# Kernel optimization log

Measured on AMD Instinct MI355X. Metric: run time of the kernel, lower is better.

## Reference

```python
import jax, jax.numpy as jnp
import numpy as np


def setup_inputs() -> dict:
    key = jax.random.key(0)
    k1, k2, k3, k4 = jax.random.split(key, 4)
    B, T, IN, D = 32, 256, 64, 128
    x = jax.random.normal(k1, (B, T, IN), dtype=jnp.float32)
    h0 = jnp.zeros((B, D), dtype=jnp.float32)
    Wx = jax.random.normal(k2, (IN, D), dtype=jnp.float32) * 0.01
    Wgate = jax.random.normal(k3, (D, D), dtype=jnp.float32) * 0.01
    Wh = jax.random.normal(k4, (D, D), dtype=jnp.float32) * 0.01
    return {"x": x, "h0": h0, "Wx": Wx, "Wgate": Wgate, "Wh": Wh}


def reference(x, h0, Wx, Wgate, Wh):
    # x: (B, T, in_dim); h0: (B, dim); returns (h_final, y, hidden_grads, dh_dWh)
    def step_single(h_r, x_r):
        # per-sample gated update: h_r (dim,), x_r (in_dim,)
        pre = x_r @ Wx + h_r @ Wh
        a = jax.nn.gelu(pre, approximate=False)  # torch GELU() is the exact erf variant
        g = jax.nn.sigmoid(a @ Wgate)
        hn = g * h_r + (1.0 - g)
        return hn, hn

    # per-step, per-sample Jacobian d h_new / d h  (mirrors vmap(jacrev(..., argnums=1)))
    jac_batched = jax.vmap(jax.jacrev(step_single, argnums=0, has_aux=True))

    def body(h, x_t):  # h: (B, dim), x_t: (B, in_dim)
        jac, h_new = jac_batched(h, x_t)  # jac: (B, dim, dim)
        return h_new, (h_new, jac)

    xt = jnp.swapaxes(x, 0, 1)  # (T, B, in_dim)
    h_final, (ys, jacs) = jax.lax.scan(body, h0, xt)
    y = jnp.swapaxes(ys, 0, 1)  # (B, T, dim)

    # last-step Jacobian wrt Wh, evaluated with the post-update h (as in the torch code)
    x_last = x[:, -1, :]

    def f_wh(Wh_):
        pre = x_last @ Wx + h_final @ Wh_
        a = jax.nn.gelu(pre, approximate=False)
        g = jax.nn.sigmoid(a @ Wgate)
        return g * h_final + (1.0 - g)

    dh_dWh = jax.jacrev(f_wh)(Wh)  # (B, dim, dim, dim)
    return (h_final, y, jacs, dh_dWh)
```

## Files before the change

### kernel.cpp

```cpp
#include <hip/hip_runtime.h>


#define JACOFF 1052672L
#define DHWOFF 135270400L

typedef __attribute__((ext_vector_type(8))) short frag_ab;
typedef __attribute__((ext_vector_type(4))) float frag_cd;

__device__ __forceinline__ short f2bf(float f) {
    unsigned u = __builtin_bit_cast(unsigned, f);
    unsigned r = (u + 0x7fffu + ((u >> 16) & 1u)) >> 16;
    return (short)r;
}

__device__ __forceinline__ void wg_barrier() {
    asm volatile("s_waitcnt lgkmcnt(0)\n\ts_barrier" ::: "memory");
}

__device__ __forceinline__ float dpp_xor1(float x) {
    int r = __builtin_amdgcn_mov_dpp(__builtin_bit_cast(int, x), 0xB1, 0xF, 0xF, true);
    return __builtin_bit_cast(float, r);
}
__device__ __forceinline__ float dpp_xor2(float x) {
    int r = __builtin_amdgcn_mov_dpp(__builtin_bit_cast(int, x), 0x4E, 0xF, 0xF, true);
    return __builtin_bit_cast(float, r);
}

__device__ __forceinline__ void gelu_pair(float pre, float& a, float& dval) {
    const float inv_sqrt2   = 0.70710678118654752f;
    const float inv_sqrt2pi = 0.39894228040143268f;
    float ex2 = __expf(-0.5f * pre * pre);
    float az  = fabsf(pre) * inv_sqrt2;
    float t   = 1.0f / (1.0f + 0.3275911f * az);
    float poly = ((((1.061405429f * t - 1.453152027f) * t + 1.421413741f) * t
                   - 0.284496736f) * t + 0.254829592f) * t;
    float erf_abs = 1.0f - poly * ex2;
    float erf_z = (pre < 0.f) ? -erf_abs : erf_abs;
    float cdf = 0.5f * (1.0f + erf_z);
    a = pre * cdf;
    dval = cdf + pre * inv_sqrt2pi * ex2;
}

__global__ __launch_bounds__(256) void prep_xw_kernel(
    const float* __restrict__ Wh, const float* __restrict__ Wg,
    const float* __restrict__ x, const float* __restrict__ Wx,
    float* __restrict__ whT, float* __restrict__ wgT, float* __restrict__ xw)
{
    int blk = blockIdx.x;
    int tid = threadIdx.x;
    if (blk < 128) {
        int idx = blk * 256 + tid;
        if (idx < 16384) {
            int k = idx >> 7, i = idx & 127;
            whT[i * 128 + k] = Wh[idx];
        } else {
            int r = idx - 16384;
            int k = r >> 7, i = r & 127;
            wgT[i * 128 + k] = Wg[r];
        }
        return;
    }
    __shared__ float xs[2][64];
    int sub = tid >> 7;
    int bt = (blk - 128) * 2 + sub;
    int i = tid & 127;
    if (i < 64) xs[sub][i] = x[bt * 64 + i];
    __syncthreads();
    float acc = 0.f;
#pragma unroll
    for (int m = 0; m < 64; ++m)
        acc += xs[sub][m] * Wx[m * 128 + i];
    xw[bt * 128 + i] = acc;
}

__global__ __launch_bounds__(512, 1) void scan_pk_kernel(
    const float* __restrict__ xw, const float* __restrict__ h0,
    const float* __restrict__ whT, const float* __restrict__ wgT,
    const float* __restrict__ Wgate, const float* __restrict__ Wh,
    float* __restrict__ out,
    short* __restrict__ Abf, float* __restrict__ wgv, float* __restrict__ wc,
    float* __restrict__ wdF, float* __restrict__ wuF, float* __restrict__ whF,
    short* __restrict__ PT)
{
    int tid = threadIdx.x;
    if (blockIdx.x >= 32) {
        int c = (blockIdx.x - 32) * 32 + (tid >> 4);
        int k0 = (tid & 15) * 8;
        int i = c >> 7, j = c & 127;
        short v[8];
#pragma unroll
        for (int m = 0; m < 8; ++m) {
            float wg = Wgate[(k0 + m) * 128 + i];
            float wh = Wh[j * 128 + k0 + m];
            v[m] = f2bf(wg * wh);
        }
        *(frag_ab*)(PT + (long)c * 128 + k0) = *(frag_ab*)v;
        return;
    }

    const int b = blockIdx.x;
    const int i = tid >> 2, qtr = tid & 3;
    __shared__ float hbuf[2][128];
    __shared__ float abuf[128];
    float wh[32], wgc[32];
    {
        const float* whr = whT + i * 128 + qtr * 32;
        const float* wgr = wgT + i * 128 + qtr * 32;
#pragma unroll
        for (int k = 0; k < 32; k += 4) {
            float4 a4 = *(const float4*)(whr + k);
            wh[k] = a4.x; wh[k + 1] = a4.y; wh[k + 2] = a4.z; wh[k + 3] = a4.w;
            float4 b4 = *(const float4*)(wgr + k);
            wgc[k] = b4.x; wgc[k + 1] = b4.y; wgc[k + 2] = b4.z; wgc[k + 3] = b4.w;
        }
    }
    if (qtr == 0) hbuf[0][i] = h0[b * 128 + i];
    __syncthreads();

    float xwv = xw[(b * 256 + 0) * 128 + i];
    float xw1 = xw[(b * 256 + 1) * 128 + i];

    for (int t = 0; t < 256; ++t) {
        int p = t & 1;
        int tn = (t < 254) ? t + 2 : 255;
        float xw2 = xw[(b * 256 + tn) * 128 + i];

        float s0 = 0.f, s1 = 0.f, s2 = 0.f, s3 = 0.f;
        const float* hb = &hbuf[p][qtr * 32];
#pragma unroll
        for (int k = 0; k < 32; k += 4) {
            float4 h4 = *(const float4*)(hb + k);
            s0 += h4.x * wh[k];
            s1 += h4.y * wh[k + 1];
            s2 += h4.z * wh[k + 2];
            s3 += h4.w * wh[k + 3];
        }
        float s = (s0 + s1) + (s2 + s3);
        s += dpp_xor1(s);
        s += dpp_xor2(s);
        float pre = xwv + s;

        float a, dval;
        gelu_pair(pre, a, dval);

        long tb = (long)(t * 32 + b) * 128 + i;
        if (qtr == 0) {
            Abf[tb] = f2bf(dval);
            abuf[i] = a;
        }
        wg_barrier();

        float r0 = 0.f, r1 = 0.f, r2 = 0.f, r3 = 0.f;
        const float* ab = &abuf[qtr * 32];
#pragma unroll
        for (int k = 0; k < 32; k += 4) {
            float4 a4 = *(const float4*)(ab + k);
            r0 += a4.x * wgc[k];
            r1 += a4.y * wgc[k + 1];
            r2 += a4.z * wgc[k + 2];
            r3 += a4.w * wgc[k + 3];
        }
        float r = (r0 + r1) + (r2 + r3);
        r += dpp_xor1(r);
        r += dpp_xor2(r);
        float g = 1.0f / (1.0f + __expf(-r));
        float hp = hbuf[p][i];
        float c = (hp - 1.0f) * g * (1.0f - g);
        float hn = g * hp + 1.0f - g;
        if (qtr == 0) {
            hbuf[p ^ 1][i] = hn;
            wgv[tb] = g;
            wc[tb] = c;
            out[4096 + (b * 256 + t) * 128 + i] = hn;
        }
        xwv = xw1; xw1 = xw2;
        wg_barrier();
    }

    float hfin = hbuf[0][i];
    if (qtr == 0) {
        out[b * 128 + i] = hfin;
        whF[b * 128 + i] = hfin;
    }

    {
        float s0 = 0.f, s1 = 0.f, s2 = 0.f, s3 = 0.f;
        const float* hb = &hbuf[0][qtr * 32];
#pragma unroll
        for (int k = 0; k < 32; k += 4) {
            float4 h4 = *(const float4*)(hb + k);
            s0 += h4.x * wh[k];
            s1 += h4.y * wh[k + 1];
            s2 += h4.z * wh[k + 2];
            s3 += h4.w * wh[k + 3];
        }
        float s = (s0 + s1) + (s2 + s3);
        s += dpp_xor1(s);
        s += dpp_xor2(s);
        float pre = xwv + s;
        float a, dval;
        gelu_pair(pre, a, dval);
        if (qtr == 0) {
            wdF[b * 128 + i] = dval;
            abuf[i] = a;
        }
        __syncthreads();
        float r0 = 0.f, r1 = 0.f, r2 = 0.f, r3 = 0.f;
        const float* ab = &abuf[qtr * 32];
#pragma unroll
        for (int k = 0; k < 32; k += 4) {
            float4 a4 = *(const float4*)(ab + k);
            r0 += a4.x * wgc[k];
            r1 += a4.y * wgc[k + 1];
            r2 += a4.z * wgc[k + 2];
            r3 += a4.w * wgc[k + 3];
        }
        float r = (r0 + r1) + (r2 + r3);
        r += dpp_xor1(r);
        r += dpp_xor2(r);
        float g = 1.0f / (1.0f + __expf(-r));
        if (qtr == 0) wuF[b * 128 + i] = (hfin - 1.0f) * g * (1.0f - g);
    }
}

__global__ __launch_bounds__(256) void jacmm_dhdw_kernel(
    const short* __restrict__ Abf,
    const short* __restrict__ PT,
    const float* __restrict__ wgv,
    const float* __restrict__ wc,
    const float* __restrict__ Wgate,
    const float* __restrict__ dF, const float* __restrict__ uF, const float* __restrict__ hF,
    float* __restrict__ out)
{
    int bx = blockIdx.x;
    int tid = threadIdx.x;
    int grp = bx / 3, rem = bx % 3;

    if (rem == 2) {
        __shared__ float hs[128], dsh[128];
        int b = grp >> 7, i = grp & 127;
        if (tid < 128) {
            hs[tid] = hF[b * 128 + tid];
            dsh[tid] = dF[b * 128 + tid];
        }
        __syncthreads();
        float u = uF[b * 128 + i];
        int q0 = (tid & 31) * 4, p0 = (tid >> 5) * 16;
        float w0 = u * dsh[q0 + 0] * Wgate[(q0 + 0) * 128 + i];
        float w1 = u * dsh[q0 + 1] * Wgate[(q0 + 1) * 128 + i];
        float w2 = u * dsh[q0 + 2] * Wgate[(q0 + 2) * 128 + i];
        float w3 = u * dsh[q0 + 3] * Wgate[(q0 + 3) * 128 + i];
        float* dst = out + DHWOFF + (long)grp * 16384;
#pragma unroll
        for (int pp = 0; pp < 16; ++pp) {
            float hp = hs[p0 + pp];
            *(float4*)(dst + (p0 + pp) * 128 + q0) = make_float4(hp * w0, hp * w1, hp * w2, hp * w3);
        }
        return;
    }

    int jb = grp * 2 + rem;
    int rb = jb & 63;
    int cb = jb >> 6;

    const short* Ag = Abf + (long)rb * (128 * 128);
    const short* Bg = PT + (long)cb * (128 * 128);

    int w = tid >> 6;
    int lane = tid & 63;
    int wr = w >> 1;
    int wcol = w & 1;
    int lrow = lane & 15;
    int quad = lane >> 4;

    long rowbase = (long)rb * 128;
    float ci[4][4], gi[4][4];
#pragma unroll
    for (int p = 0; p < 4; ++p) {
        int trow0 = wr * 64 + p * 16 + quad * 4;
#pragma unroll
        for (int reg = 0; reg < 4; ++reg) {
            long row = rowbase + trow0 + reg;
            ci[p][reg] = wc[row * 128 + cb];
            gi[p][reg] = wgv[row * 128 + cb];
        }
    }

    frag_cd acc[4][4];
#pragma unroll
    for (int p = 0; p < 4; ++p)
#pragma unroll
        for (int q = 0; q < 4; ++q) {
            acc[p][q][0] = 0.f; acc[p][q][1] = 0.f; acc[p][q][2] = 0.f; acc[p][q][3] = 0.f;
        }

#pragma unroll
    for (int kk = 0; kk < 4; ++kk) {
        int ko8 = (kk * 4 + quad) * 8;
        frag_ab af[4], bf[4];
#pragma unroll
        for (int p = 0; p < 4; ++p) {
            int r = wr * 64 + p * 16 + lrow;
            af[p] = *(const frag_ab*)(Ag + r * 128 + ko8);
        }
#pragma unroll
        for (int q = 0; q < 4; ++q) {
            int n = wcol * 64 + q * 16 + lrow;
            bf[q] = *(const frag_ab*)(Bg + n * 128 + ko8);
        }
#pragma unroll
        for (int p = 0; p < 4; ++p)
#pragma unroll
            for (int q = 0; q < 4; ++q)
                acc[p][q] = __builtin_amdgcn_mfma_f32_16x16x32_bf16(af[p], bf[q], acc[p][q], 0, 0, 0);
    }

#pragma unroll
    for (int p = 0; p < 4; ++p) {
        int trow0 = wr * 64 + p * 16 + quad * 4;
#pragma unroll
        for (int reg = 0; reg < 4; ++reg) {
            long row = rowbase + trow0 + reg;
            float* orow = out + JACOFF + row * 16384 + (long)cb * 128;
#pragma unroll
            for (int q = 0; q < 4; ++q) {
                int tcol = wcol * 64 + q * 16 + lrow;
                float v = ci[p][reg] * acc[p][q][reg];
                if (tcol == cb) v += gi[p][reg];
                orow[tcol] = v;
            }
        }
    }
}

extern "C" void kernel_launch(void* const* d_in, const int* in_sizes, int n_in,
                              void* d_out, int out_size, void* d_ws, size_t ws_size,
                              hipStream_t stream)
{
    (void)in_sizes; (void)n_in; (void)out_size; (void)ws_size;
    const float* x     = (const float*)d_in[0];
    const float* h0    = (const float*)d_in[1];
    const float* Wx    = (const float*)d_in[2];
    const float* Wgate = (const float*)d_in[3];
    const float* Wh    = (const float*)d_in[4];
    float* out = (float*)d_out;
    float* ws  = (float*)d_ws;

    float* xw  = ws;
    float* whT = ws + 1048576;
    float* wgT = ws + 1064960;
    float* wgv = ws + 1081344;
    float* wc  = ws + 2129920;
    float* wdF = ws + 3178496;
    float* wuF = ws + 3182592;
    float* whF = ws + 3186688;
    short* Abf = (short*)(ws + 3190784);
    short* PT  = (short*)(ws + 3715072);

    prep_xw_kernel<<<4224, 256, 0, stream>>>(Wh, Wgate, x, Wx, whT, wgT, xw);
    scan_pk_kernel<<<544, 512, 0, stream>>>(xw, h0, whT, wgT, Wgate, Wh, out,
                                            Abf, wgv, wc, wdF, wuF, whF, PT);
    jacmm_dhdw_kernel<<<12288, 256, 0, stream>>>(Abf, PT, wgv, wc, Wgate, wdF, wuF, whF, out);
}
```

Baseline: 1.101 ms.

## Remap recurrence matvec so each thread computes four outputs over eight-element k-slices

Changes the sequential recurrence's thread mapping. Each group of 16 threads now owns 4 output rows, and each thread covers an 8-wide k-slice. Partial sums are combined with a 16-lane DPP row reduction (row_shr 8, row_shr 4, quad perms), and xw is loaded as float4 per group. The aim is to shorten the serial per-step dependency chain and cut the shared-memory loads per thread. In exchange it adds more DPP reduction steps and more select logic.

```diff
diff --git a/kernel.cpp b/kernel.cpp
--- a/kernel.cpp
+++ b/kernel.cpp
@@ -17,13 +17,17 @@
     asm volatile("s_waitcnt lgkmcnt(0)\n\ts_barrier" ::: "memory");
 }
 
-__device__ __forceinline__ float dpp_xor1(float x) {
-    int r = __builtin_amdgcn_mov_dpp(__builtin_bit_cast(int, x), 0xB1, 0xF, 0xF, true);
-    return __builtin_bit_cast(float, r);
-}
-__device__ __forceinline__ float dpp_xor2(float x) {
-    int r = __builtin_amdgcn_mov_dpp(__builtin_bit_cast(int, x), 0x4E, 0xF, 0xF, true);
-    return __builtin_bit_cast(float, r);
+__device__ __forceinline__ float row_reduce16(float x) {
+    int t;
+    t = __builtin_amdgcn_mov_dpp(__builtin_bit_cast(int, x), 0x128, 0xF, 0xF, true);
+    x += __builtin_bit_cast(float, t);
+    t = __builtin_amdgcn_mov_dpp(__builtin_bit_cast(int, x), 0x124, 0xF, 0xF, true);
+    x += __builtin_bit_cast(float, t);
+    t = __builtin_amdgcn_mov_dpp(__builtin_bit_cast(int, x), 0x4E, 0xF, 0xF, true);
+    x += __builtin_bit_cast(float, t);
+    t = __builtin_amdgcn_mov_dpp(__builtin_bit_cast(int, x), 0xB1, 0xF, 0xF, true);
+    x += __builtin_bit_cast(float, t);
+    return x;
 }
 
 __device__ __forceinline__ void gelu_pair(float pre, float& a, float& dval) {
@@ -99,127 +103,160 @@
     }
 
     const int b = blockIdx.x;
-    const int i = tid >> 2, qtr = tid & 3;
+    const int og = tid >> 4;
+    const int kg = tid & 15;
+    const int mm = kg & 3;
+    const int iw = og * 4 + kg;
+    const bool wlane = (kg < 4);
+
     __shared__ float hbuf[2][128];
     __shared__ float abuf[128];
-    float wh[32], wgc[32];
-    {
-        const float* whr = whT + i * 128 + qtr * 32;
-        const float* wgr = wgT + i * 128 + qtr * 32;
-#pragma unroll
-        for (int k = 0; k < 32; k += 4) {
-            float4 a4 = *(const float4*)(whr + k);
-            wh[k] = a4.x; wh[k + 1] = a4.y; wh[k + 2] = a4.z; wh[k + 3] = a4.w;
-            float4 b4 = *(const float4*)(wgr + k);
-            wgc[k] = b4.x; wgc[k + 1] = b4.y; wgc[k + 2] = b4.z; wgc[k + 3] = b4.w;
-        }
-    }
-    if (qtr == 0) hbuf[0][i] = h0[b * 128 + i];
+
+    float wh[4][8], wgc[4][8];
+#pragma unroll
+    for (int m = 0; m < 4; ++m) {
+        const float* whr = whT + (og * 4 + m) * 128 + kg * 8;
+        const float* wgr = wgT + (og * 4 + m) * 128 + kg * 8;
+        float4 a4 = *(const float4*)(whr);
+        float4 b4 = *(const float4*)(whr + 4);
+        wh[m][0] = a4.x; wh[m][1] = a4.y; wh[m][2] = a4.z; wh[m][3] = a4.w;
+        wh[m][4] = b4.x; wh[m][5] = b4.y; wh[m][6] = b4.z; wh[m][7] = b4.w;
+        float4 c4 = *(const float4*)(wgr);
+        float4 d4 = *(const float4*)(wgr + 4);
+        wgc[m][0] = c4.x; wgc[m][1] = c4.y; wgc[m][2] = c4.z; wgc[m][3] = c4.w;
+        wgc[m][4] = d4.x; wgc[m][5] = d4.y; wgc[m][6] = d4.z; wgc[m][7] = d4.w;
+    }
+    if (wlane) hbuf[0][iw] = h0[b * 128 + iw];
     __syncthreads();
 
-    float xwv = xw[(b * 256 + 0) * 128 + i];
-    float xw1 = xw[(b * 256 + 1) * 128 + i];
+    float4 xwv4 = *(const float4*)(xw + (b * 256 + 0) * 128 + og * 4);
+    float4 xw14 = *(const float4*)(xw + (b * 256 + 1) * 128 + og * 4);
 
     for (int t = 0; t < 256; ++t) {
         int p = t & 1;
         int tn = (t < 254) ? t + 2 : 255;
-        float xw2 = xw[(b * 256 + tn) * 128 + i];
-
+        float4 xw24 = *(const float4*)(xw + (b * 256 + tn) * 128 + og * 4);
+
+        float h8[8];
+        {
+            const float* hb = &hbuf[p][kg * 8];
+            float4 a4 = *(const float4*)(hb);
+            float4 b4 = *(const float4*)(hb + 4);
+            h8[0] = a4.x; h8[1] = a4.y; h8[2] = a4.z; h8[3] = a4.w;
+            h8[4] = b4.x; h8[5] = b4.y; h8[6] = b4.z; h8[7] = b4.w;
+        }
         float s0 = 0.f, s1 = 0.f, s2 = 0.f, s3 = 0.f;
-        const float* hb = &hbuf[p][qtr * 32];
-#pragma unroll
-        for (int k = 0; k < 32; k += 4) {
-            float4 h4 = *(const float4*)(hb + k);
-            s0 += h4.x * wh[k];
-            s1 += h4.y * wh[k + 1];
-            s2 += h4.z * wh[k + 2];
-            s3 += h4.w * wh[k + 3];
-        }
-        float s = (s0 + s1) + (s2 + s3);
-        s += dpp_xor1(s);
-        s += dpp_xor2(s);
-        float pre = xwv + s;
-
+#pragma unroll
+        for (int kk = 0; kk < 8; ++kk) {
+            s0 += h8[kk] * wh[0][kk];
+            s1 += h8[kk] * wh[1][kk];
+            s2 += h8[kk] * wh[2][kk];
+            s3 += h8[kk] * wh[3][kk];
+        }
+        s0 = row_reduce16(s0); s1 = row_reduce16(s1);
+        s2 = row_reduce16(s2); s3 = row_reduce16(s3);
+
+        float pre = (mm == 0) ? (xwv4.x + s0) : (mm == 1) ? (xwv4.y + s1)
+                  : (mm == 2) ? (xwv4.z + s2) : (xwv4.w + s3);
         float a, dval;
         gelu_pair(pre, a, dval);
 
-        long tb = (long)(t * 32 + b) * 128 + i;
-        if (qtr == 0) {
+        long tb = (long)(t * 32 + b) * 128 + iw;
+        if (wlane) {
             Abf[tb] = f2bf(dval);
-            abuf[i] = a;
+            abuf[iw] = a;
         }
         wg_barrier();
 
+        float a8[8];
+        {
+            const float* ab = &abuf[kg * 8];
+            float4 a4 = *(const float4*)(ab);
+            float4 b4 = *(const float4*)(ab + 4);
+            a8[0] = a4.x; a8[1] = a4.y; a8[2] = a4.z; a8[3] = a4.w;
+            a8[4] = b4.x; a8[5] = b4.y; a8[6] = b4.z; a8[7] = b4.w;
+        }
         float r0 = 0.f, r1 = 0.f, r2 = 0.f, r3 = 0.f;
-        const float* ab = &abuf[qtr * 32];
-#pragma unroll
-        for (int k = 0; k < 32; k += 4) {
-            float4 a4 = *(const float4*)(ab + k);
-            r0 += a4.x * wgc[k];
-            r1 += a4.y * wgc[k + 1];
-            r2 += a4.z * wgc[k + 2];
-            r3 += a4.w * wgc[k + 3];
-        }
-        float r = (r0 + r1) + (r2 + r3);
-        r += dpp_xor1(r);
-        r += dpp_xor2(r);
+#pragma unroll
+        for (int kk = 0; kk < 8; ++kk) {
+            r0 += a8[kk] * wgc[0][kk];
+            r1 += a8[kk] * wgc[1][kk];
+            r2 += a8[kk] * wgc[2][kk];
+            r3 += a8[kk] * wgc[3][kk];
+        }
+        r0 = row_reduce16(r0); r1 = row_reduce16(r1);
+        r2 = row_reduce16(r2); r3 = row_reduce16(r3);
+        float r = (mm == 0) ? r0 : (mm == 1) ? r1 : (mm == 2) ? r2 : r3;
+
         float g = 1.0f / (1.0f + __expf(-r));
-        float hp = hbuf[p][i];
+        float hp = hbuf[p][og * 4 + mm];
         float c = (hp - 1.0f) * g * (1.0f - g);
         float hn = g * hp + 1.0f - g;
-        if (qtr == 0) {
-            hbuf[p ^ 1][i] = hn;
+        if (wlane) {
+            hbuf[p ^ 1][iw] = hn;
             wgv[tb] = g;
             wc[tb] = c;
-            out[4096 + (b * 256 + t) * 128 + i] = hn;
-        }
-        xwv = xw1; xw1 = xw2;
+            out[4096 + (b * 256 + t) * 128 + iw] = hn;
+        }
+        xwv4 = xw14; xw14 = xw24;
         wg_barrier();
     }
 
-    float hfin = hbuf[0][i];
-    if (qtr == 0) {
-        out[b * 128 + i] = hfin;
-        whF[b * 128 + i] = hfin;
+    float hfin = hbuf[0][og * 4 + mm];
+    if (wlane) {
+        out[b * 128 + iw] = hbuf[0][iw];
+        whF[b * 128 + iw] = hbuf[0][iw];
     }
 
     {
+        float h8[8];
+        {
+            const float* hb = &hbuf[0][kg * 8];
+            float4 a4 = *(const float4*)(hb);
+            float4 b4 = *(const float4*)(hb + 4);
+            h8[0] = a4.x; h8[1] = a4.y; h8[2] = a4.z; h8[3] = a4.w;
+            h8[4] = b4.x; h8[5] = b4.y; h8[6] = b4.z; h8[7] = b4.w;
+        }
         float s0 = 0.f, s1 = 0.f, s2 = 0.f, s3 = 0.f;
-        const float* hb = &hbuf[0][qtr * 32];
-#pragma unroll
-        for (int k = 0; k < 32; k += 4) {
-            float4 h4 = *(const float4*)(hb + k);
-            s0 += h4.x * wh[k];
-            s1 += h4.y * wh[k + 1];
-            s2 += h4.z * wh[k + 2];
-            s3 += h4.w * wh[k + 3];
-        }
-        float s = (s0 + s1) + (s2 + s3);
-        s += dpp_xor1(s);
-        s += dpp_xor2(s);
-        float pre = xwv + s;
+#pragma unroll
+        for (int kk = 0; kk < 8; ++kk) {
+            s0 += h8[kk] * wh[0][kk];
+            s1 += h8[kk] * wh[1][kk];
+            s2 += h8[kk] * wh[2][kk];
+            s3 += h8[kk] * wh[3][kk];
+        }
+        s0 = row_reduce16(s0); s1 = row_reduce16(s1);
+        s2 = row_reduce16(s2); s3 = row_reduce16(s3);
+        float pre = (mm == 0) ? (xwv4.x + s0) : (mm == 1) ? (xwv4.y + s1)
+                  : (mm == 2) ? (xwv4.z + s2) : (xwv4.w + s3);
         float a, dval;
         gelu_pair(pre, a, dval);
-        if (qtr == 0) {
-            wdF[b * 128 + i] = dval;
-            abuf[i] = a;
+        if (wlane) {
+            wdF[b * 128 + iw] = dval;
+            abuf[iw] = a;
         }
         __syncthreads();
+        float a8[8];
+        {
+            const float* ab = &abuf[kg * 8];
+            float4 a4 = *(const float4*)(ab);
+            float4 b4 = *(const float4*)(ab + 4);
+            a8[0] = a4.x; a8[1] = a4.y; a8[2] = a4.z; a8[3] = a4.w;
+            a8[4] = b4.x; a8[5] = b4.y; a8[6] = b4.z; a8[7] = b4.w;
+        }
         float r0 = 0.f, r1 = 0.f, r2 = 0.f, r3 = 0.f;
-        const float* ab = &abuf[qtr * 32];
-#pragma unroll
-        for (int k = 0; k < 32; k += 4) {
-            float4 a4 = *(const float4*)(ab + k);
-            r0 += a4.x * wgc[k];
-            r1 += a4.y * wgc[k + 1];
-            r2 += a4.z * wgc[k + 2];
-            r3 += a4.w * wgc[k + 3];
-        }
-        float r = (r0 + r1) + (r2 + r3);
-        r += dpp_xor1(r);
-        r += dpp_xor2(r);
+#pragma unroll
+        for (int kk = 0; kk < 8; ++kk) {
+            r0 += a8[kk] * wgc[0][kk];
+            r1 += a8[kk] * wgc[1][kk];
+            r2 += a8[kk] * wgc[2][kk];
+            r3 += a8[kk] * wgc[3][kk];
+        }
+        r0 = row_reduce16(r0); r1 = row_reduce16(r1);
+        r2 = row_reduce16(r2); r3 = row_reduce16(r3);
+        float r = (mm == 0) ? r0 : (mm == 1) ? r1 : (mm == 2) ? r2 : r3;
         float g = 1.0f / (1.0f + __expf(-r));
-        if (qtr == 0) wuF[b * 128 + i] = (hfin - 1.0f) * g * (1.0f - g);
+        if (wlane) wuF[b * 128 + iw] = (hfin - 1.0f) * g * (1.0f - g);
     }
 }
 
```

New measurement: 1.096 ms. No clear change (-0.4%).
